# Kernel optimization log

Measured on AMD Instinct MI355X. Metric: run time of the kernel, lower is better.

## Reference

```python
import jax, jax.numpy as jnp
import numpy as np

# static config (matches init_kwargs / input_specs)
T, B, CIN, H, W = 48, 64, 1, 64, 64
OC, KH, KW, STRIDE = 16, 7, 7, 2
N, P = 1000, 4
ALPHA, BETA, TH = 0.9, 0.9, 1.0
HO = (H - KH) // STRIDE + 1  # 29
WO = (W - KW) // STRIDE + 1  # 29
IN_SZ = OC * HO * WO         # 13456
SURR_ALPHA = 2.0             # snntorch default ATan surrogate alpha


@jax.custom_vjp
def atan_spike(x):
    # Heaviside forward, ATan surrogate backward (snntorch default spike_grad)
    return (x > 0).astype(x.dtype)

def _atan_fwd(x):
    return atan_spike(x), x

def _atan_bwd(x, g):
    return (g * (SURR_ALPHA / 2.0) / (1.0 + (jnp.pi / 2.0 * SURR_ALPHA * x) ** 2),)

atan_spike.defvjp(_atan_fwd, _atan_bwd)


def setup_inputs() -> dict:
    key = jax.random.key(0)
    ks = jax.random.split(key, 6)
    x = jax.random.normal(ks[0], (T, B, CIN, H, W), dtype=jnp.float32)
    gabor_w = jax.random.normal(ks[1], (OC, CIN, KH, KW), dtype=jnp.float32) * 0.3
    Wins = jax.random.normal(ks[2], (P, N, IN_SZ), dtype=jnp.float32) * (1.0 / np.sqrt(IN_SZ))
    fc1_b = jax.random.normal(ks[3], (N,), dtype=jnp.float32) * 0.01
    Wlsm = jax.random.normal(ks[4], (N, N), dtype=jnp.float32) * (0.5 / np.sqrt(N))
    rec_b = jax.random.normal(ks[5], (N,), dtype=jnp.float32) * 0.01
    return {"x": x, "gabor_w": gabor_w, "Wins": Wins, "fc1_b": fc1_b, "Wlsm": Wlsm, "rec_b": rec_b}


def _forward(x, gabor_w, Wins, fc1_b, Wlsm, rec_b):
    # Gabor conv on all timesteps at once (conv has no recurrent dependence)
    xt = x.reshape(T * B, CIN, H, W)
    g = jax.lax.conv_general_dilated(
        xt, gabor_w, window_strides=(STRIDE, STRIDE), padding="VALID",
        dimension_numbers=("NCHW", "OIHW", "NCHW"))          # [T*B, OC, HO, WO]
    feat = g.reshape(P, T // P, B, IN_SZ)
    curr = jnp.einsum("ptbi,pni->ptbn", feat, Wins).reshape(T, B, N) + fc1_b

    # RSynaptic recurrence (snntorch, reset_mechanism='subtract'):
    #   reset = H(mem_prev - th)            (detached)
    #   syn   = alpha*syn + curr + V @ spk_prev + b
    #   mem   = beta*mem + syn - reset*th
    #   spk   = H(mem - th)                 (ATan surrogate grad)
    def step(state, c):
        spk, syn, mem = state
        reset = jax.lax.stop_gradient((mem - TH > 0).astype(mem.dtype))
        syn = ALPHA * syn + c + spk @ Wlsm.T + rec_b
        mem = BETA * mem + syn - reset * TH
        spk = atan_spike(mem - TH)
        return (spk, syn, mem), spk

    z = jnp.zeros((B, N), dtype=curr.dtype)
    _, spk_rec = jax.lax.scan(step, (z, z, z), curr)
    return spk_rec  # [T, B, N]


def reference(x, gabor_w, Wins, fc1_b, Wlsm, rec_b):
    return _forward(x, gabor_w, Wins, fc1_b, Wlsm, rec_b)
```

## Files before the change

kernel.cpp:

```cpp
#include <hip/hip_runtime.h>
#include <hip/hip_bf16.h>

#define T_STEPS 48
#define B_SZ    64
#define H_IN    64
#define W_IN    64
#define OC      16
#define KH      7
#define KW      7
#define STRIDEC 2
#define HO      29
#define WO      29
#define IN_SZ   13456
#define N_NEU   1000
#define N_PAD   1024

#define WT_OFF    0ull
#define CURR_OFF  4096000ull
#define SYN_OFF   16678912ull
#define MEM_OFF   16941056ull
#define MASK_OFF  17203200ull
#define G_OFF     17219584ull

__global__ __launch_bounds__(256) void transpose_wlsm(const float* __restrict__ Wlsm,
                                                      float* __restrict__ WT) {
  __shared__ float t[32][33];
  const int m0 = blockIdx.x * 32;
  const int n0 = blockIdx.y * 32;
  const int tx = threadIdx.x & 31, ty = threadIdx.x >> 5;
  #pragma unroll
  for (int j = 0; j < 4; ++j) {
    int n = n0 + ty + j * 8, m = m0 + tx;
    t[ty + j * 8][tx] = (n < N_NEU && m < N_NEU) ? Wlsm[n * N_NEU + m] : 0.f;
  }
  __syncthreads();
  #pragma unroll
  for (int j = 0; j < 4; ++j) {
    int m = m0 + ty + j * 8, n = n0 + tx;
    if (m < N_NEU) WT[(size_t)m * N_PAD + n] = t[tx][ty + j * 8];
  }
}

__global__ __launch_bounds__(256) void conv_kernel(const float* __restrict__ x,
                                                   const float* __restrict__ w,
                                                   float* __restrict__ g,
                                                   int img0) {
  __shared__ float img[H_IN * W_IN];
  const int blk = blockIdx.x;
  const float* xim = x + (size_t)(img0 + blk) * (H_IN * W_IN);
  for (int i = threadIdx.x; i < (H_IN * W_IN) / 4; i += 256)
    ((float4*)img)[i] = ((const float4*)xim)[i];
  __syncthreads();
  float* gout = g + (size_t)blk * IN_SZ;
  for (int pos = threadIdx.x; pos < HO * WO; pos += 256) {
    const int oh = pos / WO, ow = pos - oh * WO;
    const int ih = oh * STRIDEC, iw = ow * STRIDEC;
    float acc[OC];
    #pragma unroll
    for (int oc = 0; oc < OC; ++oc) acc[oc] = 0.f;
    #pragma unroll
    for (int kh = 0; kh < KH; ++kh) {
      #pragma unroll
      for (int kw = 0; kw < KW; ++kw) {
        const float v = img[(ih + kh) * W_IN + iw + kw];
        const int widx = kh * KW + kw;
        #pragma unroll
        for (int oc = 0; oc < OC; ++oc)
          acc[oc] += v * w[oc * (KH * KW) + widx];
      }
    }
    #pragma unroll
    for (int oc = 0; oc < OC; ++oc)
      gout[oc * (HO * WO) + pos] = acc[oc];
  }
}

#define BM5 64
#define BN5 64
#define BK5 32
#define LDA5 68
#define LDB5 68
__global__ __launch_bounds__(256) void gemm_kernel(const float* __restrict__ A,
                                                   int row_off,
                                                   const float* __restrict__ Wins,
                                                   const float* __restrict__ fc1_b,
                                                   float* __restrict__ curr) {
  __shared__ __align__(16) float As[BK5 * LDA5];
  __shared__ __align__(16) float Bs[BK5 * LDB5];
  const int tid = threadIdx.x;
  const int n0 = blockIdx.x * BN5;
  const int row_l0 = blockIdx.y * BM5;
  const int r0 = (tid >> 4) * 4;
  const int c0 = (tid & 15) * 4;
  const int p = (row_off + row_l0) / 768;
  const float* Bp = Wins + (size_t)p * N_NEU * IN_SZ;

  float acc[4][4];
  #pragma unroll
  for (int i = 0; i < 4; ++i)
    #pragma unroll
    for (int j = 0; j < 4; ++j) acc[i][j] = 0.f;

  for (int k0 = 0; k0 < IN_SZ; k0 += BK5) {
    #pragma unroll
    for (int it = 0; it < 2; ++it) {
      const int f = it * 256 + tid;
      const int rr = f >> 3;
      const int kq = (f & 7) * 4;
      const int k = k0 + kq;
      float4 va = make_float4(0.f, 0.f, 0.f, 0.f);
      if (k < IN_SZ)
        va = *(const float4*)(A + (size_t)(row_l0 + rr) * IN_SZ + k);
      As[(kq + 0) * LDA5 + rr] = va.x;
      As[(kq + 1) * LDA5 + rr] = va.y;
      As[(kq + 2) * LDA5 + rr] = va.z;
      As[(kq + 3) * LDA5 + rr] = va.w;
    }
    #pragma unroll
    for (int it = 0; it < 2; ++it) {
      const int f = it * 256 + tid;
      const int cc = f >> 3;
      const int kq = (f & 7) * 4;
      const int k = k0 + kq;
      float4 vb = make_float4(0.f, 0.f, 0.f, 0.f);
      if (k < IN_SZ && n0 + cc < N_NEU)
        vb = *(const float4*)(Bp + (size_t)(n0 + cc) * IN_SZ + k);
      Bs[(kq + 0) * LDB5 + cc] = vb.x;
      Bs[(kq + 1) * LDB5 + cc] = vb.y;
      Bs[(kq + 2) * LDB5 + cc] = vb.z;
      Bs[(kq + 3) * LDB5 + cc] = vb.w;
    }
    __syncthreads();

    float lacc[4][4];
    #pragma unroll
    for (int i = 0; i < 4; ++i)
      #pragma unroll
      for (int j = 0; j < 4; ++j) lacc[i][j] = 0.f;
    #pragma unroll
    for (int kk = 0; kk < BK5; ++kk) {
      const float4 a0 = *(const float4*)&As[kk * LDA5 + r0];
      const float4 b0 = *(const float4*)&Bs[kk * LDB5 + c0];
      const float a[4] = {a0.x, a0.y, a0.z, a0.w};
      const float bb[4] = {b0.x, b0.y, b0.z, b0.w};
      #pragma unroll
      for (int i = 0; i < 4; ++i)
        #pragma unroll
        for (int j = 0; j < 4; ++j) lacc[i][j] += a[i] * bb[j];
    }
    #pragma unroll
    for (int i = 0; i < 4; ++i)
      #pragma unroll
      for (int j = 0; j < 4; ++j) acc[i][j] += lacc[i][j];
    __syncthreads();
  }

  const int g_row_base = row_off + row_l0 + r0;
  #pragma unroll
  for (int i = 0; i < 4; ++i) {
    float* crow = curr + ((size_t)(g_row_base + i) << 10);
    float4 o;
    const int nn = n0 + c0;
    o.x = acc[i][0] + fc1_b[nn + 0 < N_NEU ? nn + 0 : (N_NEU - 1)];
    o.y = acc[i][1] + fc1_b[nn + 1 < N_NEU ? nn + 1 : (N_NEU - 1)];
    o.z = acc[i][2] + fc1_b[nn + 2 < N_NEU ? nn + 2 : (N_NEU - 1)];
    o.w = acc[i][3] + fc1_b[nn + 3 < N_NEU ? nn + 3 : (N_NEU - 1)];
    *(float4*)(crow + nn) = o;
  }
}

__global__ __launch_bounds__(256) void step_kernel(
    const float* __restrict__ WT, const float* __restrict__ curr_t,
    const float* __restrict__ rec_b, float* __restrict__ syn,
    float* __restrict__ mem_s, const unsigned long long* __restrict__ mask_rd,
    unsigned long long* __restrict__ mask_wr, float* __restrict__ out_t) {
  __shared__ int idxs[1024];
  __shared__ int cnts[16];
  __shared__ int offs[17];
  __shared__ float4 red[256];
  __shared__ unsigned char nib[32];
  const int tid = threadIdx.x;
  const int b = blockIdx.x >> 3;
  const int e = blockIdx.x & 7;

  if (tid < 16) cnts[tid] = (int)__popcll(mask_rd[(b << 4) | tid]);
  __syncthreads();
  if (tid == 0) {
    int o = 0;
    #pragma unroll
    for (int c = 0; c < 16; ++c) { offs[c] = o; o += cnts[c]; }
    offs[16] = o;
  }
  __syncthreads();
  if (tid < 16) {
    unsigned long long s = mask_rd[(b << 4) | tid];
    int o = offs[tid];
    const int base = tid << 6;
    while (s) {
      idxs[o++] = base + __builtin_ctzll(s);
      s &= s - 1;
    }
  }
  __syncthreads();
  const int L = offs[16];

  const int g = tid >> 5;
  const int ln = tid & 31;
  const float* wc = WT + e * 128 + ln * 4;
  float4 acc = make_float4(0.f, 0.f, 0.f, 0.f);
  int j = g;
  for (; j + 32 <= L; j += 32) {
    const float4 v0 = *(const float4*)(wc + ((size_t)idxs[j] << 10));
    const float4 v1 = *(const float4*)(wc + ((size_t)idxs[j + 8] << 10));
    const float4 v2 = *(const float4*)(wc + ((size_t)idxs[j + 16] << 10));
    const float4 v3 = *(const float4*)(wc + ((size_t)idxs[j + 24] << 10));
    acc.x += v0.x; acc.y += v0.y; acc.z += v0.z; acc.w += v0.w;
    acc.x += v1.x; acc.y += v1.y; acc.z += v1.z; acc.w += v1.w;
    acc.x += v2.x; acc.y += v2.y; acc.z += v2.z; acc.w += v2.w;
    acc.x += v3.x; acc.y += v3.y; acc.z += v3.z; acc.w += v3.w;
  }
  for (; j + 16 <= L; j += 16) {
    const float4 v0 = *(const float4*)(wc + ((size_t)idxs[j] << 10));
    const float4 v1 = *(const float4*)(wc + ((size_t)idxs[j + 8] << 10));
    acc.x += v0.x; acc.y += v0.y; acc.z += v0.z; acc.w += v0.w;
    acc.x += v1.x; acc.y += v1.y; acc.z += v1.z; acc.w += v1.w;
  }
  for (; j < L; j += 8) {
    const float4 v = *(const float4*)(wc + ((size_t)idxs[j] << 10));
    acc.x += v.x; acc.y += v.y; acc.z += v.z; acc.w += v.w;
  }
  red[tid] = acc;
  __syncthreads();

  if (tid < 32) {
    float4 rec = red[tid];
    #pragma unroll
    for (int h = 1; h < 8; ++h) {
      const float4 v = red[h * 32 + tid];
      rec.x += v.x; rec.y += v.y; rec.z += v.z; rec.w += v.w;
    }
    const int n = e * 128 + tid * 4;
    const size_t idx = ((size_t)b << 10) + n;
    const float4 cv = *(const float4*)(curr_t + idx);
    float4 sv = *(float4*)(syn + idx);
    float4 mv = *(float4*)(mem_s + idx);
    const float rb0 = (n + 0 < N_NEU) ? rec_b[n + 0] : 0.f;
    const float rb1 = (n + 1 < N_NEU) ? rec_b[n + 1] : 0.f;
    const float rb2 = (n + 2 < N_NEU) ? rec_b[n + 2] : 0.f;
    const float rb3 = (n + 3 < N_NEU) ? rec_b[n + 3] : 0.f;
    float4 sn, mn;
    sn.x = 0.9f * sv.x + cv.x + rec.x + rb0;
    sn.y = 0.9f * sv.y + cv.y + rec.y + rb1;
    sn.z = 0.9f * sv.z + cv.z + rec.z + rb2;
    sn.w = 0.9f * sv.w + cv.w + rec.w + rb3;
    mn.x = 0.9f * mv.x + sn.x - ((mv.x - 1.0f > 0.f) ? 1.0f : 0.f);
    mn.y = 0.9f * mv.y + sn.y - ((mv.y - 1.0f > 0.f) ? 1.0f : 0.f);
    mn.z = 0.9f * mv.z + sn.z - ((mv.z - 1.0f > 0.f) ? 1.0f : 0.f);
    mn.w = 0.9f * mv.w + sn.w - ((mv.w - 1.0f > 0.f) ? 1.0f : 0.f);
    *(float4*)(syn + idx) = sn;
    *(float4*)(mem_s + idx) = mn;
    const int s0 = ((mn.x - 1.0f) > 0.f && n + 0 < N_NEU) ? 1 : 0;
    const int s1 = ((mn.y - 1.0f) > 0.f && n + 1 < N_NEU) ? 1 : 0;
    const int s2 = ((mn.z - 1.0f) > 0.f && n + 2 < N_NEU) ? 1 : 0;
    const int s3 = ((mn.w - 1.0f) > 0.f && n + 3 < N_NEU) ? 1 : 0;
    if (n + 0 < N_NEU) out_t[b * N_NEU + n + 0] = (float)s0;
    if (n + 1 < N_NEU) out_t[b * N_NEU + n + 1] = (float)s1;
    if (n + 2 < N_NEU) out_t[b * N_NEU + n + 2] = (float)s2;
    if (n + 3 < N_NEU) out_t[b * N_NEU + n + 3] = (float)s3;
    nib[tid] = (unsigned char)(s0 | (s1 << 1) | (s2 << 2) | (s3 << 3));
  }
  __syncthreads();
  if (tid < 2) {
    unsigned long long w = 0;
    #pragma unroll
    for (int i = 0; i < 16; ++i)
      w |= (unsigned long long)nib[tid * 16 + i] << (4 * i);
    mask_wr[(b << 4) | (e * 2 + tid)] = w;
  }
}

extern "C" void kernel_launch(void* const* d_in, const int* in_sizes, int n_in,
                              void* d_out, int out_size, void* d_ws, size_t ws_size,
                              hipStream_t stream) {
  const float* x     = (const float*)d_in[0];
  const float* gw    = (const float*)d_in[1];
  const float* Wins  = (const float*)d_in[2];
  const float* fc1_b = (const float*)d_in[3];
  const float* Wlsm  = (const float*)d_in[4];
  const float* rec_b = (const float*)d_in[5];
  float* out = (float*)d_out;
  char* ws = (char*)d_ws;

  float* WT   = (float*)(ws + WT_OFF);
  float* curr = (float*)(ws + CURR_OFF);
  float* syn  = (float*)(ws + SYN_OFF);
  float* mem  = (float*)(ws + MEM_OFF);
  unsigned long long* mask = (unsigned long long*)(ws + MASK_OFF);
  float* gbuf = (float*)(ws + G_OFF);

  (void)hipMemsetAsync(ws + SYN_OFF, 0, (size_t)(MASK_OFF - SYN_OFF) + 16384, stream);

  hipLaunchKernelGGL(transpose_wlsm, dim3(32, 32), dim3(256), 0, stream, Wlsm, WT);

  const size_t needA = G_OFF + (size_t)3072 * IN_SZ * 4;
  if (ws_size >= needA) {
    hipLaunchKernelGGL(conv_kernel, dim3(3072), dim3(256), 0, stream, x, gw, gbuf, 0);
    hipLaunchKernelGGL(gemm_kernel, dim3(16, 48), dim3(256), 0, stream,
                       gbuf, 0, Wins, fc1_b, curr);
  } else {
    for (int p = 0; p < 4; ++p) {
      hipLaunchKernelGGL(conv_kernel, dim3(768), dim3(256), 0, stream,
                         x, gw, gbuf, p * 768);
      hipLaunchKernelGGL(gemm_kernel, dim3(16, 12), dim3(256), 0, stream,
                         gbuf, p * 768, Wins, fc1_b, curr);
    }
  }

  for (int t = 0; t < T_STEPS; ++t) {
    hipLaunchKernelGGL(step_kernel, dim3(512), dim3(256), 0, stream,
                       WT, curr + (size_t)t * 65536, rec_b, syn, mem,
                       mask + (size_t)(t & 1) * 1024,
                       mask + (size_t)((t + 1) & 1) * 1024,
                       out + (size_t)t * 64000);
  }
}
```

Baseline: 2.536 ms.

## Fuse all recurrent timesteps into one persistent kernel per batch row

Replaces the 48 per-timestep step_kernel launches with a single kernel that has one 1024-thread block per batch element. That block loops over all timesteps, keeping syn and mem in registers and the spike mask in shared memory built with a wavefront ballot. This removes 47 kernel launches, the global syn/mem/mask round trips and the workspace memset. In exchange only 64 blocks run on the whole GPU, and each thread does the sparse recurrent gather alone with scalar loads instead of splitting it across 8 blocks per batch, so the gather parallelism per batch drops.

```diff
diff --git a/kernel.cpp b/kernel.cpp
--- a/kernel.cpp
+++ b/kernel.cpp
@@ -169,113 +169,79 @@
   }
 }
 
-__global__ __launch_bounds__(256) void step_kernel(
-    const float* __restrict__ WT, const float* __restrict__ curr_t,
-    const float* __restrict__ rec_b, float* __restrict__ syn,
-    float* __restrict__ mem_s, const unsigned long long* __restrict__ mask_rd,
-    unsigned long long* __restrict__ mask_wr, float* __restrict__ out_t) {
+__global__ __launch_bounds__(1024) void steps_fused(
+    const float* __restrict__ WT, const float* __restrict__ curr,
+    const float* __restrict__ rec_b, float* __restrict__ out) {
+  __shared__ unsigned long long smask[16];
   __shared__ int idxs[1024];
   __shared__ int cnts[16];
   __shared__ int offs[17];
-  __shared__ float4 red[256];
-  __shared__ unsigned char nib[32];
   const int tid = threadIdx.x;
-  const int b = blockIdx.x >> 3;
-  const int e = blockIdx.x & 7;
-
-  if (tid < 16) cnts[tid] = (int)__popcll(mask_rd[(b << 4) | tid]);
-  __syncthreads();
-  if (tid == 0) {
-    int o = 0;
-    #pragma unroll
-    for (int c = 0; c < 16; ++c) { offs[c] = o; o += cnts[c]; }
-    offs[16] = o;
-  }
-  __syncthreads();
-  if (tid < 16) {
-    unsigned long long s = mask_rd[(b << 4) | tid];
-    int o = offs[tid];
-    const int base = tid << 6;
-    while (s) {
-      idxs[o++] = base + __builtin_ctzll(s);
-      s &= s - 1;
-    }
-  }
-  __syncthreads();
-  const int L = offs[16];
-
-  const int g = tid >> 5;
-  const int ln = tid & 31;
-  const float* wc = WT + e * 128 + ln * 4;
-  float4 acc = make_float4(0.f, 0.f, 0.f, 0.f);
-  int j = g;
-  for (; j + 32 <= L; j += 32) {
-    const float4 v0 = *(const float4*)(wc + ((size_t)idxs[j] << 10));
-    const float4 v1 = *(const float4*)(wc + ((size_t)idxs[j + 8] << 10));
-    const float4 v2 = *(const float4*)(wc + ((size_t)idxs[j + 16] << 10));
-    const float4 v3 = *(const float4*)(wc + ((size_t)idxs[j + 24] << 10));
-    acc.x += v0.x; acc.y += v0.y; acc.z += v0.z; acc.w += v0.w;
-    acc.x += v1.x; acc.y += v1.y; acc.z += v1.z; acc.w += v1.w;
-    acc.x += v2.x; acc.y += v2.y; acc.z += v2.z; acc.w += v2.w;
-    acc.x += v3.x; acc.y += v3.y; acc.z += v3.z; acc.w += v3.w;
-  }
-  for (; j + 16 <= L; j += 16) {
-    const float4 v0 = *(const float4*)(wc + ((size_t)idxs[j] << 10));
-    const float4 v1 = *(const float4*)(wc + ((size_t)idxs[j + 8] << 10));
-    acc.x += v0.x; acc.y += v0.y; acc.z += v0.z; acc.w += v0.w;
-    acc.x += v1.x; acc.y += v1.y; acc.z += v1.z; acc.w += v1.w;
-  }
-  for (; j < L; j += 8) {
-    const float4 v = *(const float4*)(wc + ((size_t)idxs[j] << 10));
-    acc.x += v.x; acc.y += v.y; acc.z += v.z; acc.w += v.w;
-  }
-  red[tid] = acc;
-  __syncthreads();
-
-  if (tid < 32) {
-    float4 rec = red[tid];
-    #pragma unroll
-    for (int h = 1; h < 8; ++h) {
-      const float4 v = red[h * 32 + tid];
-      rec.x += v.x; rec.y += v.y; rec.z += v.z; rec.w += v.w;
-    }
-    const int n = e * 128 + tid * 4;
-    const size_t idx = ((size_t)b << 10) + n;
-    const float4 cv = *(const float4*)(curr_t + idx);
-    float4 sv = *(float4*)(syn + idx);
-    float4 mv = *(float4*)(mem_s + idx);
-    const float rb0 = (n + 0 < N_NEU) ? rec_b[n + 0] : 0.f;
-    const float rb1 = (n + 1 < N_NEU) ? rec_b[n + 1] : 0.f;
-    const float rb2 = (n + 2 < N_NEU) ? rec_b[n + 2] : 0.f;
-    const float rb3 = (n + 3 < N_NEU) ? rec_b[n + 3] : 0.f;
-    float4 sn, mn;
-    sn.x = 0.9f * sv.x + cv.x + rec.x + rb0;
-    sn.y = 0.9f * sv.y + cv.y + rec.y + rb1;
-    sn.z = 0.9f * sv.z + cv.z + rec.z + rb2;
-    sn.w = 0.9f * sv.w + cv.w + rec.w + rb3;
-    mn.x = 0.9f * mv.x + sn.x - ((mv.x - 1.0f > 0.f) ? 1.0f : 0.f);
-    mn.y = 0.9f * mv.y + sn.y - ((mv.y - 1.0f > 0.f) ? 1.0f : 0.f);
-    mn.z = 0.9f * mv.z + sn.z - ((mv.z - 1.0f > 0.f) ? 1.0f : 0.f);
-    mn.w = 0.9f * mv.w + sn.w - ((mv.w - 1.0f > 0.f) ? 1.0f : 0.f);
-    *(float4*)(syn + idx) = sn;
-    *(float4*)(mem_s + idx) = mn;
-    const int s0 = ((mn.x - 1.0f) > 0.f && n + 0 < N_NEU) ? 1 : 0;
-    const int s1 = ((mn.y - 1.0f) > 0.f && n + 1 < N_NEU) ? 1 : 0;
-    const int s2 = ((mn.z - 1.0f) > 0.f && n + 2 < N_NEU) ? 1 : 0;
-    const int s3 = ((mn.w - 1.0f) > 0.f && n + 3 < N_NEU) ? 1 : 0;
-    if (n + 0 < N_NEU) out_t[b * N_NEU + n + 0] = (float)s0;
-    if (n + 1 < N_NEU) out_t[b * N_NEU + n + 1] = (float)s1;
-    if (n + 2 < N_NEU) out_t[b * N_NEU + n + 2] = (float)s2;
-    if (n + 3 < N_NEU) out_t[b * N_NEU + n + 3] = (float)s3;
-    nib[tid] = (unsigned char)(s0 | (s1 << 1) | (s2 << 2) | (s3 << 3));
-  }
-  __syncthreads();
-  if (tid < 2) {
-    unsigned long long w = 0;
-    #pragma unroll
-    for (int i = 0; i < 16; ++i)
-      w |= (unsigned long long)nib[tid * 16 + i] << (4 * i);
-    mask_wr[(b << 4) | (e * 2 + tid)] = w;
+  const int b = blockIdx.x;
+  const int n = tid;
+  const int wid = tid >> 6, lane = tid & 63;
+  float syn = 0.f, mem = 0.f;
+  const float rbv = (n < N_NEU) ? rec_b[n] : 0.f;
+  const float* wtn = WT + n;
+  if (tid < 16) smask[tid] = 0ull;
+
+  for (int t = 0; t < T_STEPS; ++t) {
+    __syncthreads();
+    if (tid < 16) cnts[tid] = (int)__popcll(smask[tid]);
+    __syncthreads();
+    if (tid == 0) {
+      int o = 0;
+      #pragma unroll
+      for (int c = 0; c < 16; ++c) { offs[c] = o; o += cnts[c]; }
+      offs[16] = o;
+    }
+    __syncthreads();
+    if (tid < 16) {
+      unsigned long long s = smask[tid];
+      int o = offs[tid];
+      const int base = tid << 6;
+      while (s) {
+        idxs[o++] = base + __builtin_ctzll(s);
+        s &= s - 1;
+      }
+    }
+    __syncthreads();
+    const int L = offs[16];
+
+    float p0 = 0.f, p1 = 0.f, p2 = 0.f, p3 = 0.f;
+    float p4 = 0.f, p5 = 0.f, p6 = 0.f, p7 = 0.f;
+    int j = 0;
+    for (; j + 8 <= L; j += 8) {
+      const int m0 = idxs[j + 0], m1 = idxs[j + 1], m2 = idxs[j + 2], m3 = idxs[j + 3];
+      const int m4 = idxs[j + 4], m5 = idxs[j + 5], m6 = idxs[j + 6], m7 = idxs[j + 7];
+      p0 += wtn[(size_t)m0 << 10];
+      p1 += wtn[(size_t)m1 << 10];
+      p2 += wtn[(size_t)m2 << 10];
+      p3 += wtn[(size_t)m3 << 10];
+      p4 += wtn[(size_t)m4 << 10];
+      p5 += wtn[(size_t)m5 << 10];
+      p6 += wtn[(size_t)m6 << 10];
+      p7 += wtn[(size_t)m7 << 10];
+    }
+    const int rem = L - j;
+    if (rem > 0) p0 += wtn[(size_t)idxs[j + 0] << 10];
+    if (rem > 1) p1 += wtn[(size_t)idxs[j + 1] << 10];
+    if (rem > 2) p2 += wtn[(size_t)idxs[j + 2] << 10];
+    if (rem > 3) p3 += wtn[(size_t)idxs[j + 3] << 10];
+    if (rem > 4) p4 += wtn[(size_t)idxs[j + 4] << 10];
+    if (rem > 5) p5 += wtn[(size_t)idxs[j + 5] << 10];
+    if (rem > 6) p6 += wtn[(size_t)idxs[j + 6] << 10];
+    float rec = p0;
+    rec += p1; rec += p2; rec += p3; rec += p4; rec += p5; rec += p6; rec += p7;
+
+    const float cv = curr[((size_t)t << 16) + ((size_t)b << 10) + n];
+    syn = 0.9f * syn + cv + rec + rbv;
+    const float reset = (mem - 1.0f > 0.f) ? 1.0f : 0.f;
+    mem = 0.9f * mem + syn - reset;
+    const int spk = ((mem - 1.0f) > 0.f && n < N_NEU) ? 1 : 0;
+    if (n < N_NEU) out[(size_t)t * 64000 + b * 1000 + n] = (float)spk;
+    const unsigned long long bal = __ballot(spk);
+    if (lane == 0) smask[wid] = bal;
   }
 }
 
@@ -293,12 +259,7 @@
 
   float* WT   = (float*)(ws + WT_OFF);
   float* curr = (float*)(ws + CURR_OFF);
-  float* syn  = (float*)(ws + SYN_OFF);
-  float* mem  = (float*)(ws + MEM_OFF);
-  unsigned long long* mask = (unsigned long long*)(ws + MASK_OFF);
   float* gbuf = (float*)(ws + G_OFF);
-
-  (void)hipMemsetAsync(ws + SYN_OFF, 0, (size_t)(MASK_OFF - SYN_OFF) + 16384, stream);
 
   hipLaunchKernelGGL(transpose_wlsm, dim3(32, 32), dim3(256), 0, stream, Wlsm, WT);
 
@@ -316,11 +277,6 @@
     }
   }
 
-  for (int t = 0; t < T_STEPS; ++t) {
-    hipLaunchKernelGGL(step_kernel, dim3(512), dim3(256), 0, stream,
-                       WT, curr + (size_t)t * 65536, rec_b, syn, mem,
-                       mask + (size_t)(t & 1) * 1024,
-                       mask + (size_t)((t + 1) & 1) * 1024,
-                       out + (size_t)t * 64000);
-  }
-}
+  hipLaunchKernelGGL(steps_fused, dim3(64), dim3(1024), 0, stream,
+                     WT, curr, rec_b, out);
+}
```

Measured after the change: 4.168 ms. 64.3% more time.
